# Performance work log

Hardware: AMD Instinct MI355X
Metric: run time of the kernel (lower is better)

## Reference

```python
import jax, jax.numpy as jnp
import numpy as np

N_NODES = 100000
N_EDGES = 1600000
NUM_RELS = 200
NUM_BASES = 4
IN_FEAT = 20   # hardcoded by `view(-1, 1, 20)` in the torch source
OUT_FEAT = 20
SUBMAT_IN = IN_FEAT // NUM_BASES   # 5
SUBMAT_OUT = OUT_FEAT // NUM_BASES # 5


def setup_inputs() -> dict:
    key = jax.random.key(0)
    ks = jax.random.split(key, 9)
    return {
        "h": jax.random.normal(ks[0], (N_NODES, IN_FEAT), dtype=jnp.float32),
        "weight": jax.random.normal(ks[1], (NUM_RELS, NUM_BASES * SUBMAT_IN * SUBMAT_OUT), dtype=jnp.float32),
        "bias_term": jax.random.normal(ks[2], (NUM_RELS, OUT_FEAT), dtype=jnp.float32),
        "gate_weight": jax.random.normal(ks[3], (NUM_RELS, OUT_FEAT, 1), dtype=jnp.float32),
        "gate_bias": jax.random.normal(ks[4], (NUM_RELS, 1), dtype=jnp.float32),
        "loop_weight": jax.random.normal(ks[5], (IN_FEAT, OUT_FEAT), dtype=jnp.float32),
        "edge_src": jax.random.randint(ks[6], (N_EDGES,), 0, N_NODES, dtype=jnp.int32),
        "edge_dst": jax.random.randint(ks[7], (N_EDGES,), 0, N_NODES, dtype=jnp.int32),
        "etype": jax.random.randint(ks[8], (NUM_RELS,), 0, NUM_RELS, dtype=jnp.int32) if False else jax.random.randint(ks[8], (N_EDGES,), 0, NUM_RELS, dtype=jnp.int32),
    }


def reference(h, weight, bias_term, gate_weight, gate_bias, loop_weight, edge_src, edge_dst, etype):
    n_nodes = h.shape[0]
    # self-loop message (dropout=0.0 -> identity)
    loop_message = h @ loop_weight                                    # [N, out]
    # per-edge relation-indexed gathers
    W = weight[etype].reshape(-1, NUM_BASES, SUBMAT_IN, SUBMAT_OUT)   # [E, B, si, so]
    src = h[edge_src]                                                 # [E, in]
    node = src.reshape(-1, NUM_BASES, SUBMAT_IN)                      # [E, B, si]
    # block-diagonal small matmul
    msg = jnp.einsum('ebi,ebio->ebo', node, W).reshape(-1, OUT_FEAT)  # [E, out]
    # gate: sigmoid(<full src node, gate_weight_r> + gate_bias_r)
    gw = gate_weight[etype, :, 0]                                     # [E, out(=20=in)]
    gb = gate_bias[etype, 0]                                          # [E]
    gate = jax.nn.sigmoid(jnp.sum(src * gw, axis=-1) + gb)            # [E]
    msg = gate[:, None] * (msg + bias_term[etype])                    # [E, out]
    # scatter-sum aggregation to destination nodes (zero init for isolated nodes)
    agg = jax.ops.segment_sum(msg, edge_dst, num_segments=n_nodes)    # [N, out]
    return jax.nn.relu(agg + loop_message)
```

## Files before the change

### kernel.cpp

```cpp
#include <hip/hip_runtime.h>
#include <hip/hip_fp16.h>
#include <math.h>

#define IN_FEAT 20
#define OUT_FEAT 20
#define NUM_BASES 4
#define SUBMAT_IN 5
#define SUBMAT_OUT 5
#define NUM_RELS 200
#define CAP 64
#define NPB 160
#define BCAP 3072
#define EPB 4096


__global__ void __launch_bounds__(1024)
prep_kernel(const float* __restrict__ h, __half* __restrict__ h_pad,
            const int* __restrict__ edge_src,
            const int* __restrict__ edge_dst,
            const int* __restrict__ etype,
            int* __restrict__ cursor,
            int2* __restrict__ bucketed,
            int n_nodes, int n_edges, int nb, int nsb) {
    __shared__ int  lhist[640];
    __shared__ int  lofs[640];
    __shared__ int  lrank[640];
    __shared__ int  lbase[640];
    __shared__ int  lws[16];
    __shared__ int2 img[EPB];
    int tid = threadIdx.x;

    if (blockIdx.x >= nsb) {
        int v = (blockIdx.x - nsb) * 1024 + tid;
        if (v >= n_nodes) return;
        const float4* hp = (const float4*)(h + (size_t)v * IN_FEAT);
        float4 a = hp[0], b = hp[1], c = hp[2], d = hp[3], e = hp[4];
        __half2 p0 = __floats2half2_rn(a.x, a.y), p1 = __floats2half2_rn(a.z, a.w);
        __half2 p2 = __floats2half2_rn(b.x, b.y), p3 = __floats2half2_rn(b.z, b.w);
        __half2 p4 = __floats2half2_rn(c.x, c.y), p5 = __floats2half2_rn(c.z, c.w);
        __half2 p6 = __floats2half2_rn(d.x, d.y), p7 = __floats2half2_rn(d.z, d.w);
        __half2 p8 = __floats2half2_rn(e.x, e.y), p9 = __floats2half2_rn(e.z, e.w);
        uint4 w0, w1; uint2 w2;
        w0.x = *(unsigned*)&p0; w0.y = *(unsigned*)&p1; w0.z = *(unsigned*)&p2; w0.w = *(unsigned*)&p3;
        w1.x = *(unsigned*)&p4; w1.y = *(unsigned*)&p5; w1.z = *(unsigned*)&p6; w1.w = *(unsigned*)&p7;
        w2.x = *(unsigned*)&p8; w2.y = *(unsigned*)&p9;
        char* dst = (char*)(h_pad + (size_t)v * 32);
        *(uint4*)(dst)      = w0;
        *(uint4*)(dst + 16) = w1;
        *(uint2*)(dst + 32) = w2;
        return;
    }

    for (int i = tid; i < nb; i += 1024) { lhist[i] = 0; lrank[i] = 0; }
    __syncthreads();

    int blockbase = blockIdx.x * EPB;
    int e0 = blockbase + tid * 4;
    int s[4], d[4], t[4], bk[4];
    bool val[4];
    if (e0 + 3 < n_edges) {
        int4 sv = *(const int4*)(edge_src + e0);
        int4 dv = *(const int4*)(edge_dst + e0);
        int4 tv = *(const int4*)(etype + e0);
        s[0]=sv.x; s[1]=sv.y; s[2]=sv.z; s[3]=sv.w;
        d[0]=dv.x; d[1]=dv.y; d[2]=dv.z; d[3]=dv.w;
        t[0]=tv.x; t[1]=tv.y; t[2]=tv.z; t[3]=tv.w;
        val[0]=val[1]=val[2]=val[3]=true;
    } else {
#pragma unroll
        for (int k = 0; k < 4; ++k) {
            int e = e0 + k;
            val[k] = (e < n_edges);
            s[k] = val[k] ? edge_src[e] : 0;
            d[k] = val[k] ? edge_dst[e] : 0;
            t[k] = val[k] ? etype[e] : 0;
        }
    }
#pragma unroll
    for (int k = 0; k < 4; ++k) {
        bk[k] = d[k] / NPB;
        if (val[k]) atomicAdd(&lhist[bk[k]], 1);
    }
    __syncthreads();

    int hv = (tid < nb) ? lhist[tid] : 0;
    int x = hv;
#pragma unroll
    for (int s2 = 1; s2 < 64; s2 <<= 1) {
        int y = __shfl_up(x, s2, 64);
        if ((tid & 63) >= s2) x += y;
    }
    if ((tid & 63) == 63) lws[tid >> 6] = x;
    __syncthreads();
    if (tid < 16) {
        int w = lws[tid];
#pragma unroll
        for (int s2 = 1; s2 < 16; s2 <<= 1) {
            int y = __shfl_up(w, s2, 16);
            if (tid >= s2) w += y;
        }
        lws[tid] = w;
    }
    __syncthreads();
    int wb = (tid >> 6) ? lws[(tid >> 6) - 1] : 0;
    if (tid < nb) {
        lofs[tid] = wb + x - hv;
        if (hv > 0) lbase[tid] = atomicAdd(&cursor[tid], hv);
    }
    __syncthreads();

#pragma unroll
    for (int k = 0; k < 4; ++k) {
        if (val[k]) {
            int r = atomicAdd(&lrank[bk[k]], 1);
            unsigned packed = (unsigned)s[k] | ((unsigned)t[k] << 17);
            img[lofs[bk[k]] + r] = make_int2(d[k], (int)packed);
        }
    }
    __syncthreads();

    int m = n_edges - blockbase; if (m > EPB) m = EPB;
    for (int i = tid; i < m; i += 1024) {
        int2 e = img[i];
        int b2 = e.x / NPB;
        int dst = lbase[b2] + (i - lofs[b2]);
        if (dst < BCAP) bucketed[(size_t)b2 * BCAP + dst] = e;
    }
}

__global__ void __launch_bounds__(1024)
place_csr_kernel(const int* __restrict__ cursor,
                 const int2* __restrict__ bucketed,
                 unsigned* __restrict__ records,
                 int* __restrict__ cnt,
                 int* __restrict__ off,
                 int n_nodes, int nb) {
    __shared__ int2 simg[BCAP];
    __shared__ int  rws[16];
    __shared__ int  pws[4];
    __shared__ int  lcnt[NPB];
    __shared__ int  sscan[NPB];
    __shared__ int  lrank[NPB];
    int b = blockIdx.x, tid = threadIdx.x;
    int node0 = b * NPB;

    int rv = (tid < b && tid < nb) ? min(cursor[tid], BCAP) : 0;
#pragma unroll
    for (int s2 = 32; s2 > 0; s2 >>= 1) rv += __shfl_xor(rv, s2, 64);
    if ((tid & 63) == 0) rws[tid >> 6] = rv;
    if (tid < NPB) { lcnt[tid] = 0; lrank[tid] = 0; }
    __syncthreads();
    if (tid == 0) {
        int s = 0;
#pragma unroll
        for (int k = 0; k < 16; ++k) s += rws[k];
        rws[0] = s;
    }
    __syncthreads();
    int gbase = rws[0];

    int m = cursor[b]; if (m > BCAP) m = BCAP;

    for (int i = tid; i < m; i += 1024) {
        int2 r = bucketed[(size_t)b * BCAP + i];
        simg[i] = r;
        atomicAdd(&lcnt[r.x - node0], 1);
    }
    __syncthreads();

    int cv = (tid < NPB) ? lcnt[tid] : 0;
    int x = cv;
#pragma unroll
    for (int s2 = 1; s2 < 64; s2 <<= 1) {
        int y = __shfl_up(x, s2, 64);
        if ((tid & 63) >= s2) x += y;
    }
    if ((tid & 63) == 63 && (tid >> 6) < 3) pws[tid >> 6] = x;
    __syncthreads();
    if (tid < 4) {
        int w = (tid < 3) ? pws[tid] : 0;
#pragma unroll
        for (int s2 = 1; s2 < 4; s2 <<= 1) {
            int y = __shfl_up(w, s2, 4);
            if (tid >= s2) w += y;
        }
        pws[tid] = w;
    }
    __syncthreads();
    if (tid < NPB) {
        int wb = (tid >> 6) ? pws[(tid >> 6) - 1] : 0;
        int excl = wb + x - cv;
        int v = node0 + tid;
        if (v < n_nodes) { cnt[v] = cv; off[v] = gbase + excl; }
        sscan[tid] = excl;
    }
    __syncthreads();

    for (int i = tid; i < m; i += 1024) {
        int2 r = simg[i];
        int dl = r.x - node0;
        int rk = atomicAdd(&lrank[dl], 1);
        records[(size_t)gbase + sscan[dl] + rk] = (unsigned)r.y;
    }
}

__global__ void __launch_bounds__(1024, 4)
gather_kernel(const float* __restrict__ h,
              const __half* __restrict__ h_pad,
              const float* __restrict__ loop_weight,
              const float* __restrict__ weight,
              const float* __restrict__ bias_term,
              const float* __restrict__ gate_weight,
              const float* __restrict__ gate_bias,
              const int* __restrict__ cnt,
              const int* __restrict__ off,
              const unsigned* __restrict__ records,
              float* __restrict__ out, int n_nodes, int n_groups) {
    __shared__ __half2 lds_wp[NUM_RELS * 51];
    __shared__ float   lds_gwt[IN_FEAT * NUM_RELS];
    __shared__ float   lds_gb[NUM_RELS];
    __shared__ float   lds_lw[IN_FEAT * OUT_FEAT];
    int tid = threadIdx.x;
    for (int idx = tid; idx < NUM_RELS * 50; idx += 1024) {
        int t = idx / 50, f = idx - t * 50;
        lds_wp[t * 51 + f] = __floats2half2_rn(weight[t * 100 + f],
                                               weight[t * 100 + f + 50]);
    }
    for (int idx = tid; idx < IN_FEAT * NUM_RELS; idx += 1024) {
        int t = idx / IN_FEAT, i = idx - t * IN_FEAT;
        lds_gwt[i * NUM_RELS + t] = gate_weight[idx];
    }
    for (int idx = tid; idx < NUM_RELS; idx += 1024) lds_gb[idx] = gate_bias[idx];
    for (int idx = tid; idx < IN_FEAT * OUT_FEAT; idx += 1024) lds_lw[idx] = loop_weight[idx];
    __syncthreads();

    int wave = blockIdx.x * 16 + (tid >> 6);
    int nwaves = gridDim.x * 16;
    int l = tid & 63;
    int l16 = l & 15;

    for (int grp = wave; grp < n_groups; grp += nwaves) {
        int v = grp * 4 + (l >> 4);
        bool valid = (v < n_nodes);
        int c = 0, base = 0;
        if (valid) { c = cnt[v]; base = off[v]; }
        if (c > CAP) c = CAP;

        float acc[OUT_FEAT];
#pragma unroll
        for (int j = 0; j < OUT_FEAT; ++j) acc[j] = 0.0f;

        if (valid) {
#pragma unroll
            for (int i0 = 0; i0 < 2; ++i0) {
                int i = l16 + i0 * 16;
                if (i < IN_FEAT) {
                    float s = h[(size_t)v * IN_FEAT + i];
#pragma unroll
                    for (int j = 0; j < OUT_FEAT; ++j)
                        acc[j] = fmaf(s, lds_lw[i * OUT_FEAT + j], acc[j]);
                }
            }
        }

#pragma unroll
        for (int it = 0; it < 4; ++it) {
            int slot = l16 + it * 16;
            if (valid && slot < c) {
                unsigned p = records[(size_t)base + slot];
                int srcid = (int)(p & 0x1FFFFu);
                int t = (int)(p >> 17);

                const char* sp = (const char*)(h_pad + (size_t)srcid * 32);
                uint4 A = *(const uint4*)(sp);
                uint4 B = *(const uint4*)(sp + 16);
                uint2 C = *(const uint2*)(sp + 32);
                float src[IN_FEAT];
                {
                    unsigned u[10] = {A.x, A.y, A.z, A.w, B.x, B.y, B.z, B.w, C.x, C.y};
#pragma unroll
                    for (int q = 0; q < 10; ++q) {
                        __half2 hv = *reinterpret_cast<__half2*>(&u[q]);
                        float2 f = __half22float2(hv);
                        src[2 * q] = f.x; src[2 * q + 1] = f.y;
                    }
                }

                float g = lds_gb[t];
#pragma unroll
                for (int i = 0; i < IN_FEAT; ++i)
                    g = fmaf(src[i], lds_gwt[i * NUM_RELS + t], g);
                g = 1.0f / (1.0f + __expf(-g));

#pragma unroll
                for (int i = 0; i < IN_FEAT; ++i) src[i] *= g;

                const __half2* wp = lds_wp + t * 51;
#pragma unroll
                for (int f = 0; f < 50; ++f) {
                    float2 w = __half22float2(wp[f]);
                    const int b0 = f / 25, r = f - b0 * 25;
                    const int i0 = r / 5, o0 = r - i0 * 5;
                    acc[b0 * 5 + o0] =
                        fmaf(src[b0 * 5 + i0], w.x, acc[b0 * 5 + o0]);
                    acc[(b0 + 2) * 5 + o0] =
                        fmaf(src[(b0 + 2) * 5 + i0], w.y, acc[(b0 + 2) * 5 + o0]);
                }

                const float4* btp = (const float4*)(bias_term + (size_t)t * OUT_FEAT);
#pragma unroll
                for (int k = 0; k < OUT_FEAT / 4; ++k) {
                    float4 bv = btp[k];
                    acc[4 * k + 0] = fmaf(g, bv.x, acc[4 * k + 0]);
                    acc[4 * k + 1] = fmaf(g, bv.y, acc[4 * k + 1]);
                    acc[4 * k + 2] = fmaf(g, bv.z, acc[4 * k + 2]);
                    acc[4 * k + 3] = fmaf(g, bv.w, acc[4 * k + 3]);
                }
            }
        }

#pragma unroll
        for (int mask = 8; mask > 0; mask >>= 1) {
#pragma unroll
            for (int j = 0; j < OUT_FEAT; ++j)
                acc[j] += __shfl_xor(acc[j], mask, 16);
        }

        if (valid && l16 < OUT_FEAT / 4) {
            float4 tv;
            tv.x = fmaxf(acc[4 * l16 + 0], 0.0f);
            tv.y = fmaxf(acc[4 * l16 + 1], 0.0f);
            tv.z = fmaxf(acc[4 * l16 + 2], 0.0f);
            tv.w = fmaxf(acc[4 * l16 + 3], 0.0f);
            ((float4*)(out + (size_t)v * OUT_FEAT))[l16] = tv;
        }
    }
}

__global__ void loop_msg_kernel(const float* __restrict__ h,
                                const float* __restrict__ loop_weight,
                                float* __restrict__ out, int n_nodes) {
    int v = blockIdx.x * blockDim.x + threadIdx.x;
    if (v >= n_nodes) return;
    float src[IN_FEAT];
    const float4* hp = (const float4*)(h + (size_t)v * IN_FEAT);
#pragma unroll
    for (int i = 0; i < IN_FEAT / 4; ++i) {
        float4 t = hp[i];
        src[4 * i + 0] = t.x; src[4 * i + 1] = t.y;
        src[4 * i + 2] = t.z; src[4 * i + 3] = t.w;
    }
    float acc[OUT_FEAT];
#pragma unroll
    for (int j = 0; j < OUT_FEAT; ++j) acc[j] = 0.0f;
#pragma unroll
    for (int i = 0; i < IN_FEAT; ++i) {
        float s = src[i];
#pragma unroll
        for (int j = 0; j < OUT_FEAT; ++j)
            acc[j] = fmaf(s, loop_weight[i * OUT_FEAT + j], acc[j]);
    }
    float4* op = (float4*)(out + (size_t)v * OUT_FEAT);
#pragma unroll
    for (int j = 0; j < OUT_FEAT / 4; ++j) {
        float4 t;
        t.x = acc[4 * j + 0]; t.y = acc[4 * j + 1];
        t.z = acc[4 * j + 2]; t.w = acc[4 * j + 3];
        op[j] = t;
    }
}

__global__ void edge_atomic_kernel(const float* __restrict__ h,
                                   const float* __restrict__ weight,
                                   const float* __restrict__ bias_term,
                                   const float* __restrict__ gate_weight,
                                   const float* __restrict__ gate_bias,
                                   const int* __restrict__ edge_src,
                                   const int* __restrict__ edge_dst,
                                   const int* __restrict__ etype,
                                   float* __restrict__ out, int n_edges) {
    int e = blockIdx.x * blockDim.x + threadIdx.x;
    if (e >= n_edges) return;
    int s = edge_src[e], d = edge_dst[e], t = etype[e];
    float src[IN_FEAT];
    const float4* hp = (const float4*)(h + (size_t)s * IN_FEAT);
#pragma unroll
    for (int i = 0; i < IN_FEAT / 4; ++i) {
        float4 v = hp[i];
        src[4 * i + 0] = v.x; src[4 * i + 1] = v.y;
        src[4 * i + 2] = v.z; src[4 * i + 3] = v.w;
    }
    const float* W = weight + (size_t)t * 100;
    float msg[OUT_FEAT];
#pragma unroll
    for (int j = 0; j < OUT_FEAT; ++j) msg[j] = 0.0f;
#pragma unroll
    for (int b = 0; b < NUM_BASES; ++b)
#pragma unroll
        for (int i = 0; i < SUBMAT_IN; ++i) {
            float sv = src[b * SUBMAT_IN + i];
#pragma unroll
            for (int o = 0; o < SUBMAT_OUT; ++o)
                msg[b * SUBMAT_OUT + o] =
                    fmaf(sv, W[(b * SUBMAT_IN + i) * SUBMAT_OUT + o],
                         msg[b * SUBMAT_OUT + o]);
        }
    const float* gw = gate_weight + (size_t)t * OUT_FEAT;
    float g = gate_bias[t];
#pragma unroll
    for (int i = 0; i < IN_FEAT; ++i) g = fmaf(src[i], gw[i], g);
    g = 1.0f / (1.0f + __expf(-g));
    const float* bt = bias_term + (size_t)t * OUT_FEAT;
    float* dstp = out + (size_t)d * OUT_FEAT;
#pragma unroll
    for (int j = 0; j < OUT_FEAT; ++j) atomicAdd(&dstp[j], g * (msg[j] + bt[j]));
}

__global__ void relu_kernel(float* __restrict__ out, int n4) {
    int i = blockIdx.x * blockDim.x + threadIdx.x;
    if (i >= n4) return;
    float4* p = (float4*)out;
    float4 v = p[i];
    v.x = fmaxf(v.x, 0.0f); v.y = fmaxf(v.y, 0.0f);
    v.z = fmaxf(v.z, 0.0f); v.w = fmaxf(v.w, 0.0f);
    p[i] = v;
}

extern "C" void kernel_launch(void* const* d_in, const int* in_sizes, int n_in,
                              void* d_out, int out_size, void* d_ws, size_t ws_size,
                              hipStream_t stream) {
    const float* h           = (const float*)d_in[0];
    const float* weight      = (const float*)d_in[1];
    const float* bias_term   = (const float*)d_in[2];
    const float* gate_weight = (const float*)d_in[3];
    const float* gate_bias   = (const float*)d_in[4];
    const float* loop_weight = (const float*)d_in[5];
    const int* edge_src      = (const int*)d_in[6];
    const int* edge_dst      = (const int*)d_in[7];
    const int* etype         = (const int*)d_in[8];
    float* out = (float*)d_out;

    const int n_nodes = in_sizes[0] / IN_FEAT;
    const int n_edges = in_sizes[6];
    const int nb = (n_nodes + NPB - 1) / NPB;
    const int nsb = (n_edges + EPB - 1) / EPB;
    const int hb = (n_nodes + 1023) / 1024;

    size_t off_cursor   = 0;
    size_t off_bucketed = (((size_t)nb * 4 + 127) / 128) * 128;
    size_t off_records  = ((off_bucketed + (size_t)nb * BCAP * 8 + 127) / 128) * 128;
    size_t off_cnt      = ((off_records + (size_t)n_edges * 4 + 127) / 128) * 128;
    size_t off_offs     = ((off_cnt + (size_t)n_nodes * 4 + 127) / 128) * 128;
    size_t off_hpad     = ((off_offs + (size_t)n_nodes * 4 + 127) / 128) * 128;
    size_t need = off_hpad + (size_t)n_nodes * 64;

    bool ok = (ws_size >= need) && (n_nodes <= (1 << 17)) && (nb <= 1024) &&
              (in_sizes[4] == NUM_RELS) && (in_sizes[1] == NUM_RELS * 100) &&
              (in_sizes[5] == IN_FEAT * OUT_FEAT);

    if (ok) {
        int*  cursor      = (int*)((char*)d_ws + off_cursor);
        int2* bucketed    = (int2*)((char*)d_ws + off_bucketed);
        unsigned* records = (unsigned*)((char*)d_ws + off_records);
        int*  cnt         = (int*)((char*)d_ws + off_cnt);
        int*  off         = (int*)((char*)d_ws + off_offs);
        __half* h_pad     = (__half*)((char*)d_ws + off_hpad);

        hipMemsetAsync(cursor, 0, (size_t)nb * sizeof(int), stream);
        prep_kernel<<<nsb + hb, 1024, 0, stream>>>(
            h, h_pad, edge_src, edge_dst, etype, cursor, bucketed,
            n_nodes, n_edges, nb, nsb);
        place_csr_kernel<<<nb, 1024, 0, stream>>>(
            cursor, bucketed, records, cnt, off, n_nodes, nb);
        int n_groups = (n_nodes + 3) / 4;
        gather_kernel<<<512, 1024, 0, stream>>>(
            h, h_pad, loop_weight, weight, bias_term, gate_weight, gate_bias,
            cnt, off, records, out, n_nodes, n_groups);
    } else {
        loop_msg_kernel<<<(n_nodes + 255) / 256, 256, 0, stream>>>(
            h, loop_weight, out, n_nodes);
        edge_atomic_kernel<<<(n_edges + 255) / 256, 256, 0, stream>>>(
            h, weight, bias_term, gate_weight, gate_bias,
            edge_src, edge_dst, etype, out, n_edges);
        relu_kernel<<<(n_nodes * OUT_FEAT / 4 + 255) / 256, 256, 0, stream>>>(
            out, n_nodes * OUT_FEAT / 4);
    }
}
```

Before: 199.9 us.

## Use packed fp16 dot and FMA for per-edge gate and message math

Node features in h_pad are reordered so each half2 packs features i and i+10. That lets the gate be computed with 10 packed fp16 dot2 ops and the block-diagonal message with 50 packed half2 FMAs instead of about 100 scalar fp32 FMAs. Gate weights and bias_term are staged in LDS as interleaved half2 arrays, replacing the global float4 bias loads per edge. The goal is to cut per-edge ALU work and fp16-to-fp32 conversions. In exchange, each edge's message is now accumulated in fp16, which adds rounding error.

Result: faster. 190.1 us (-4.9%).

```diff
diff --git a/kernel.cpp b/kernel.cpp
--- a/kernel.cpp
+++ b/kernel.cpp
@@ -1,6 +1,7 @@
 #include <hip/hip_runtime.h>
 #include <hip/hip_fp16.h>
 #include <math.h>
+#include <string.h>
 
 #define IN_FEAT 20
 #define OUT_FEAT 20
@@ -13,6 +14,24 @@
 #define BCAP 3072
 #define EPB 4096
 
+
+typedef _Float16 v2h __attribute__((ext_vector_type(2)));
+
+__device__ __forceinline__ float fdot2u(unsigned a, __half2 b, float c) {
+#if __has_builtin(__builtin_amdgcn_fdot2)
+    union { unsigned u; v2h v; } ca; ca.u = a;
+    union { __half2 h; v2h v; } cb; cb.h = b;
+    return __builtin_amdgcn_fdot2(ca.v, cb.v, c, false);
+#else
+    union { unsigned u; __half2 h; } ca; ca.u = a;
+    float2 fa = __half22float2(ca.h), fb = __half22float2(b);
+    return fmaf(fa.x, fb.x, fmaf(fa.y, fb.y, c));
+#endif
+}
+
+__device__ __forceinline__ __half2 u2h2(unsigned x) {
+    union { unsigned u; __half2 h; } c; c.u = x; return c.h;
+}
 
 __global__ void __launch_bounds__(1024)
 prep_kernel(const float* __restrict__ h, __half* __restrict__ h_pad,
@@ -35,11 +54,16 @@
         if (v >= n_nodes) return;
         const float4* hp = (const float4*)(h + (size_t)v * IN_FEAT);
         float4 a = hp[0], b = hp[1], c = hp[2], d = hp[3], e = hp[4];
-        __half2 p0 = __floats2half2_rn(a.x, a.y), p1 = __floats2half2_rn(a.z, a.w);
-        __half2 p2 = __floats2half2_rn(b.x, b.y), p3 = __floats2half2_rn(b.z, b.w);
-        __half2 p4 = __floats2half2_rn(c.x, c.y), p5 = __floats2half2_rn(c.z, c.w);
-        __half2 p6 = __floats2half2_rn(d.x, d.y), p7 = __floats2half2_rn(d.z, d.w);
-        __half2 p8 = __floats2half2_rn(e.x, e.y), p9 = __floats2half2_rn(e.z, e.w);
+        __half2 p0 = __floats2half2_rn(a.x, c.z);
+        __half2 p1 = __floats2half2_rn(a.y, c.w);
+        __half2 p2 = __floats2half2_rn(a.z, d.x);
+        __half2 p3 = __floats2half2_rn(a.w, d.y);
+        __half2 p4 = __floats2half2_rn(b.x, d.z);
+        __half2 p5 = __floats2half2_rn(b.y, d.w);
+        __half2 p6 = __floats2half2_rn(b.z, e.x);
+        __half2 p7 = __floats2half2_rn(b.w, e.y);
+        __half2 p8 = __floats2half2_rn(c.x, e.z);
+        __half2 p9 = __floats2half2_rn(c.y, e.w);
         uint4 w0, w1; uint2 w2;
         w0.x = *(unsigned*)&p0; w0.y = *(unsigned*)&p1; w0.z = *(unsigned*)&p2; w0.w = *(unsigned*)&p3;
         w1.x = *(unsigned*)&p4; w1.y = *(unsigned*)&p5; w1.z = *(unsigned*)&p6; w1.w = *(unsigned*)&p7;
@@ -217,7 +241,8 @@
               const unsigned* __restrict__ records,
               float* __restrict__ out, int n_nodes, int n_groups) {
     __shared__ __half2 lds_wp[NUM_RELS * 51];
-    __shared__ float   lds_gwt[IN_FEAT * NUM_RELS];
+    __shared__ __half2 lds_gw2[10 * 201];
+    __shared__ __half2 lds_bt2[10 * 201];
     __shared__ float   lds_gb[NUM_RELS];
     __shared__ float   lds_lw[IN_FEAT * OUT_FEAT];
     int tid = threadIdx.x;
@@ -226,9 +251,12 @@
         lds_wp[t * 51 + f] = __floats2half2_rn(weight[t * 100 + f],
                                                weight[t * 100 + f + 50]);
     }
-    for (int idx = tid; idx < IN_FEAT * NUM_RELS; idx += 1024) {
-        int t = idx / IN_FEAT, i = idx - t * IN_FEAT;
-        lds_gwt[i * NUM_RELS + t] = gate_weight[idx];
+    for (int idx = tid; idx < 10 * NUM_RELS; idx += 1024) {
+        int q = idx / NUM_RELS, t = idx - q * NUM_RELS;
+        lds_gw2[q * 201 + t] = __floats2half2_rn(gate_weight[t * IN_FEAT + q],
+                                                 gate_weight[t * IN_FEAT + q + 10]);
+        lds_bt2[q * 201 + t] = __floats2half2_rn(bias_term[t * OUT_FEAT + q],
+                                                 bias_term[t * OUT_FEAT + q + 10]);
     }
     for (int idx = tid; idx < NUM_RELS; idx += 1024) lds_gb[idx] = gate_bias[idx];
     for (int idx = tid; idx < IN_FEAT * OUT_FEAT; idx += 1024) lds_lw[idx] = loop_weight[idx];
@@ -275,46 +303,39 @@
                 uint4 A = *(const uint4*)(sp);
                 uint4 B = *(const uint4*)(sp + 16);
                 uint2 C = *(const uint2*)(sp + 32);
-                float src[IN_FEAT];
-                {
-                    unsigned u[10] = {A.x, A.y, A.z, A.w, B.x, B.y, B.z, B.w, C.x, C.y};
-#pragma unroll
-                    for (int q = 0; q < 10; ++q) {
-                        __half2 hv = *reinterpret_cast<__half2*>(&u[q]);
-                        float2 f = __half22float2(hv);
-                        src[2 * q] = f.x; src[2 * q + 1] = f.y;
-                    }
+                unsigned u[10] = {A.x, A.y, A.z, A.w, B.x, B.y, B.z, B.w, C.x, C.y};
+
+                float g = lds_gb[t];
+#pragma unroll
+                for (int q = 0; q < 10; ++q)
+                    g = fdot2u(u[q], lds_gw2[q * 201 + t], g);
+                g = 1.0f / (1.0f + __expf(-g));
+                __half2 g2 = __float2half2_rn(g);
+
+                __half2 s2[10];
+#pragma unroll
+                for (int q = 0; q < 10; ++q) s2[q] = __hmul2(u2h2(u[q]), g2);
+
+                __half2 m2[10];
+#pragma unroll
+                for (int q = 0; q < 10; ++q)
+                    m2[q] = __hmul2(lds_bt2[q * 201 + t], g2);
+
+                const __half2* wp = lds_wp + t * 51;
+#pragma unroll
+                for (int f = 0; f < 50; ++f) {
+                    const int r  = f / 5;
+                    const int o  = f - r * 5;
+                    const int b0 = r / 5;
+                    const int pp = b0 * 5 + o;
+                    m2[pp] = __hfma2(s2[r], wp[f], m2[pp]);
                 }
 
-                float g = lds_gb[t];
-#pragma unroll
-                for (int i = 0; i < IN_FEAT; ++i)
-                    g = fmaf(src[i], lds_gwt[i * NUM_RELS + t], g);
-                g = 1.0f / (1.0f + __expf(-g));
-
-#pragma unroll
-                for (int i = 0; i < IN_FEAT; ++i) src[i] *= g;
-
-                const __half2* wp = lds_wp + t * 51;
-#pragma unroll
-                for (int f = 0; f < 50; ++f) {
-                    float2 w = __half22float2(wp[f]);
-                    const int b0 = f / 25, r = f - b0 * 25;
-                    const int i0 = r / 5, o0 = r - i0 * 5;
-                    acc[b0 * 5 + o0] =
-                        fmaf(src[b0 * 5 + i0], w.x, acc[b0 * 5 + o0]);
-                    acc[(b0 + 2) * 5 + o0] =
-                        fmaf(src[(b0 + 2) * 5 + i0], w.y, acc[(b0 + 2) * 5 + o0]);
-                }
-
-                const float4* btp = (const float4*)(bias_term + (size_t)t * OUT_FEAT);
-#pragma unroll
-                for (int k = 0; k < OUT_FEAT / 4; ++k) {
-                    float4 bv = btp[k];
-                    acc[4 * k + 0] = fmaf(g, bv.x, acc[4 * k + 0]);
-                    acc[4 * k + 1] = fmaf(g, bv.y, acc[4 * k + 1]);
-                    acc[4 * k + 2] = fmaf(g, bv.z, acc[4 * k + 2]);
-                    acc[4 * k + 3] = fmaf(g, bv.w, acc[4 * k + 3]);
+#pragma unroll
+                for (int q = 0; q < 10; ++q) {
+                    float2 fm = __half22float2(m2[q]);
+                    acc[q]      += fm.x;
+                    acc[q + 10] += fm.y;
                 }
             }
         }
```
